# Performance work log

Hardware: AMD Instinct MI355X
Metric: run time of the kernel (lower is better)

Reference implementation:

```python
import jax, jax.numpy as jnp
import numpy as np

N = 8192
IN_F = 512
OUT_F = 256
ALPHA = 0.2          # LeakyReLU negative slope
MASK_VAL = -9e15     # same sentinel as the torch code


def setup_inputs() -> dict:
    key = jax.random.key(0)
    k1, k2, k3, k4, k5, k6 = jax.random.split(key, 6)
    inputs = jax.random.normal(k1, (N, IN_F), dtype=jnp.float32)
    # sparse-ish 0/1 dense adjacency (~avg degree 64)
    adj = (jax.random.uniform(k2, (N, N)) < (64.0 / N)).astype(jnp.float32)
    W = jax.random.normal(k3, (IN_F, OUT_F), dtype=jnp.float32) * (1.414 / np.sqrt(IN_F))
    a = jax.random.normal(k4, (2 * OUT_F, 1), dtype=jnp.float32) * 0.1
    W_gc = jax.random.normal(k5, (IN_F, OUT_F), dtype=jnp.float32) * (1.414 / np.sqrt(IN_F))
    b_gc = jax.random.normal(k6, (OUT_F,), dtype=jnp.float32) * 0.01
    return {"inputs": inputs, "adj": adj, "W": W, "a": a, "W_gc": W_gc, "b_gc": b_gc}


def reference(inputs, adj, W, a, W_gc, b_gc):
    # h: [n, F]
    h = inputs @ W
    F = h.shape[1]
    # Fused additive attention: e[i,j] = leaky_relu(a1.h_i + a2.h_j)
    # (mathematically identical to the repeat/cat construction in the source)
    f_src = h @ a[:F, 0]   # [n]
    f_dst = h @ a[F:, 0]   # [n]
    e = jax.nn.leaky_relu(f_src[:, None] + f_dst[None, :], negative_slope=ALPHA)  # [n, n]
    # masked row-softmax over neighbors
    att = jnp.where(adj > 0, e, MASK_VAL)
    att = jax.nn.softmax(att, axis=1)
    # dropout p=0.0 -> identity
    h_prime = att @ h  # [n, F]
    # optional dense graph-convolution branch (graph_convolve=True)
    gc = adj @ (inputs @ W_gc) + b_gc
    return h_prime + gc
```

## Files before the change

kernel.cpp:

```cpp
#include <hip/hip_runtime.h>
#include <hip/hip_bf16.h>
#include <math.h>

#define N_NODES 8192
#define IN_F    512
#define OUT_F   256
#define NCAT    512
#define ALPHA   0.2f
#define MAXDEG  512

typedef __attribute__((ext_vector_type(8))) short short8;
typedef __attribute__((ext_vector_type(4))) float f32x4;

static __device__ __forceinline__ short f2bf(float f) {
    union { float f; unsigned u; } v; v.f = f;
    unsigned r = v.u + 0x7fffu + ((v.u >> 16) & 1u);
    return (short)(r >> 16);
}
static __device__ __forceinline__ float bf2f(short s) {
    union { unsigned u; float f; } v;
    v.u = ((unsigned)(unsigned short)s) << 16;
    return v.f;
}

__global__ __launch_bounds__(512) void bt_pack(const float* __restrict__ W,
                                               const float* __restrict__ W_gc,
                                               short* __restrict__ Bt) {
    const int n = blockIdx.x;
    const int k = threadIdx.x;
    const int c = n >> 1;
    float v = (n & 1) ? W_gc[(size_t)k * OUT_F + c] : W[(size_t)k * OUT_F + c];
    Bt[(size_t)n * IN_F + k] = f2bf(v);
}

__global__ __launch_bounds__(256) void gemm_mfma(const float* __restrict__ A,
                                                 const short* __restrict__ Bt,
                                                 short* __restrict__ hcat) {
    __shared__ short As[128 * 32];
    __shared__ short Bs[128 * 32];

    const int tid  = threadIdx.x;
    const int m0   = blockIdx.y * 128;
    const int n0   = blockIdx.x * 128;
    const int wid  = tid >> 6;
    const int lane = tid & 63;
    const int wr   = wid >> 1;
    const int wc   = wid & 1;
    const int mh   = lane & 15;
    const int q    = lane >> 4;

    const int srow  = tid >> 1;
    const int shalf = tid & 1;

    const f32x4 vzero = {0.f, 0.f, 0.f, 0.f};
    f32x4 acc[4][4];
    #pragma unroll
    for (int i = 0; i < 4; i++)
        #pragma unroll
        for (int j = 0; j < 4; j++) acc[i][j] = vzero;

    const float* aga = A  + (size_t)(m0 + srow) * IN_F + shalf * 16;
    const short* bgb = Bt + (size_t)(n0 + srow) * IN_F + shalf * 16;
    short* asw = &As[srow * 32 + shalf * 16];
    short* bsw = &Bs[srow * 32 + shalf * 16];

    for (int k0 = 0; k0 < IN_F; k0 += 32) {
        const float4* a4 = (const float4*)(aga + k0);
        float4 x0 = a4[0], x1 = a4[1], x2 = a4[2], x3 = a4[3];
        const int4* b4 = (const int4*)(bgb + k0);
        int4 bv0 = b4[0], bv1 = b4[1];

        short8 p0, p1;
        p0[0] = f2bf(x0.x); p0[1] = f2bf(x0.y); p0[2] = f2bf(x0.z); p0[3] = f2bf(x0.w);
        p0[4] = f2bf(x1.x); p0[5] = f2bf(x1.y); p0[6] = f2bf(x1.z); p0[7] = f2bf(x1.w);
        p1[0] = f2bf(x2.x); p1[1] = f2bf(x2.y); p1[2] = f2bf(x2.z); p1[3] = f2bf(x2.w);
        p1[4] = f2bf(x3.x); p1[5] = f2bf(x3.y); p1[6] = f2bf(x3.z); p1[7] = f2bf(x3.w);

        __syncthreads();
        *(short8*)asw       = p0;
        *(short8*)(asw + 8) = p1;
        *(int4*)bsw         = bv0;
        *(int4*)(bsw + 8)   = bv1;
        __syncthreads();

        short8 af[4], bfm[4];
        #pragma unroll
        for (int i = 0; i < 4; i++) {
            af[i]  = *(const short8*)&As[(wr * 64 + i * 16 + mh) * 32 + q * 8];
            bfm[i] = *(const short8*)&Bs[(wc * 64 + i * 16 + mh) * 32 + q * 8];
        }
        #pragma unroll
        for (int mi = 0; mi < 4; mi++)
            #pragma unroll
            for (int ni = 0; ni < 4; ni++)
                acc[mi][ni] = __builtin_amdgcn_mfma_f32_16x16x32_bf16(
                    af[mi], bfm[ni], acc[mi][ni], 0, 0, 0);
    }

    #pragma unroll
    for (int mi = 0; mi < 4; mi++)
        #pragma unroll
        for (int ni = 0; ni < 4; ni++) {
            const int col   = n0 + wc * 64 + ni * 16 + mh;
            const int rbase = m0 + wr * 64 + mi * 16 + q * 4;
            f32x4 v = acc[mi][ni];
            #pragma unroll
            for (int r = 0; r < 4; r++)
                hcat[(size_t)(rbase + r) * NCAT + col] = f2bf(v[r]);
        }
}

__global__ __launch_bounds__(256) void compute_f(const short* __restrict__ hcat,
                                                 const float* __restrict__ a,
                                                 float* __restrict__ f_src,
                                                 float* __restrict__ f_dst) {
    const int row  = blockIdx.x * 4 + (threadIdx.x >> 6);
    const int lane = threadIdx.x & 63;
    const short* hr = hcat + (size_t)row * NCAT;
    float s1 = 0.f, s2 = 0.f;
    #pragma unroll
    for (int c = lane; c < OUT_F; c += 64) {
        float hv = bf2f(hr[2 * c]);
        s1 += hv * a[c];
        s2 += hv * a[OUT_F + c];
    }
    #pragma unroll
    for (int off = 32; off; off >>= 1) {
        s1 += __shfl_down(s1, off);
        s2 += __shfl_down(s2, off);
    }
    if (lane == 0) { f_src[row] = s1; f_dst[row] = s2; }
}

__global__ __launch_bounds__(256) void attn_row(const float* __restrict__ adj,
                                                const short* __restrict__ hcat,
                                                const float* __restrict__ f_src,
                                                const float* __restrict__ f_dst,
                                                const float* __restrict__ b_gc,
                                                float* __restrict__ out) {
    __shared__ int   s_idx[MAXDEG];
    __shared__ float s_w[MAXDEG];
    __shared__ float s_red[4];
    __shared__ int   s_count;

    const int row  = blockIdx.x;
    const int tid  = threadIdx.x;
    const int lane = tid & 63;
    const int wid  = tid >> 6;

    if (tid == 0) s_count = 0;
    __syncthreads();

    const float fs = f_src[row];
    const f32x4* arow4 = (const f32x4*)(adj + (size_t)row * N_NODES);

    f32x4 v[8];
    #pragma unroll
    for (int it = 0; it < 8; it++)
        v[it] = arow4[it * 256 + tid];

    float lloc = 0.f;
    #pragma unroll
    for (int it = 0; it < 8; it++) {
        int c4 = (v[it][0] > 0.f) + (v[it][1] > 0.f) +
                 (v[it][2] > 0.f) + (v[it][3] > 0.f);
        if (c4) {
            int pos = atomicAdd(&s_count, c4);
            const int j0 = (it * 256 + tid) * 4;
            #pragma unroll
            for (int i = 0; i < 4; i++) {
                if (v[it][i] > 0.f) {
                    float e = fs + f_dst[j0 + i];
                    e = (e > 0.f) ? e : ALPHA * e;
                    float w = __expf(e);
                    s_idx[pos] = j0 + i;
                    s_w[pos]   = w;
                    pos++;
                    lloc += w;
                }
            }
        }
    }
    #pragma unroll
    for (int off = 32; off; off >>= 1) lloc += __shfl_down(lloc, off);
    if (lane == 0) s_red[wid] = lloc;
    __syncthreads();

    const int   deg   = min(s_count, MAXDEG);
    const float l     = s_red[0] + s_red[1] + s_red[2] + s_red[3];
    const float inv_l = (deg > 0) ? 1.f / l : 0.f;

    const int u = lane >> 4;
    const int p = lane & 15;
    const short* hbase = hcat + wid * 128 + p * 8;

    float aa0 = 0.f, aa1 = 0.f, aa2 = 0.f, aa3 = 0.f;
    float gg0 = 0.f, gg1 = 0.f, gg2 = 0.f, gg3 = 0.f;
    #pragma unroll 4
    for (int k = u; k < deg; k += 4) {
        const int   j = s_idx[k];
        const float w = s_w[k];
        short8 hv = *(const short8*)(hbase + (size_t)j * NCAT);
        aa0 += w * bf2f(hv[0]); gg0 += bf2f(hv[1]);
        aa1 += w * bf2f(hv[2]); gg1 += bf2f(hv[3]);
        aa2 += w * bf2f(hv[4]); gg2 += bf2f(hv[5]);
        aa3 += w * bf2f(hv[6]); gg3 += bf2f(hv[7]);
    }
    aa0 += __shfl_down(aa0, 32); aa1 += __shfl_down(aa1, 32);
    aa2 += __shfl_down(aa2, 32); aa3 += __shfl_down(aa3, 32);
    gg0 += __shfl_down(gg0, 32); gg1 += __shfl_down(gg1, 32);
    gg2 += __shfl_down(gg2, 32); gg3 += __shfl_down(gg3, 32);
    aa0 += __shfl_down(aa0, 16); aa1 += __shfl_down(aa1, 16);
    aa2 += __shfl_down(aa2, 16); aa3 += __shfl_down(aa3, 16);
    gg0 += __shfl_down(gg0, 16); gg1 += __shfl_down(gg1, 16);
    gg2 += __shfl_down(gg2, 16); gg3 += __shfl_down(gg3, 16);

    if (u == 0) {
        const int col = wid * 64 + p * 4;
        const float4 bg = *(const float4*)(b_gc + col);
        float4 o;
        o.x = aa0 * inv_l + gg0 + bg.x;
        o.y = aa1 * inv_l + gg1 + bg.y;
        o.z = aa2 * inv_l + gg2 + bg.z;
        o.w = aa3 * inv_l + gg3 + bg.w;
        *(float4*)(out + (size_t)row * OUT_F + col) = o;
    }
}

extern "C" void kernel_launch(void* const* d_in, const int* in_sizes, int n_in,
                              void* d_out, int out_size, void* d_ws, size_t ws_size,
                              hipStream_t stream) {
    const float* inputs = (const float*)d_in[0];
    const float* adj    = (const float*)d_in[1];
    const float* W      = (const float*)d_in[2];
    const float* a      = (const float*)d_in[3];
    const float* W_gc   = (const float*)d_in[4];
    const float* b_gc   = (const float*)d_in[5];
    float* out = (float*)d_out;

    short* Bt    = (short*)d_ws;
    short* hcat  = Bt + (size_t)NCAT * IN_F;
    float* f_src = (float*)(hcat + (size_t)N_NODES * NCAT);
    float* f_dst = f_src + N_NODES;

    bt_pack<<<dim3(NCAT), dim3(IN_F), 0, stream>>>(W, W_gc, Bt);
    gemm_mfma<<<dim3(NCAT / 128, N_NODES / 128), 256, 0, stream>>>(inputs, Bt, hcat);
    compute_f<<<N_NODES / 4, 256, 0, stream>>>(hcat, a, f_src, f_dst);
    attn_row<<<N_NODES, 256, 0, stream>>>(adj, hcat, f_src, f_dst, b_gc, out);
}
```

Baseline: 424.1 us.

## Pre-pack inputs to bf16, shrink GEMM tiles, split attention weight pass, batch gathers

Adds a separate pass that converts the inputs to bf16 before the GEMM. The GEMM tile shrinks from 128x128 to 64x64, giving more blocks, and bt_pack is rewritten so its reads are coalesced. compute_f now does one vectorized load per lane. In attn_row, neighbor indices are collected first and the exp weights are computed in a separate balanced pass, so the per-thread divergent work goes away. The gather loop also issues 8 independent row loads at a time to hide latency. The costs are an extra kernel launch, extra memory traffic for the bf16 copy of the inputs, and less operand reuse per GEMM tile.

```diff
diff --git a/kernel.cpp b/kernel.cpp
--- a/kernel.cpp
+++ b/kernel.cpp
@@ -23,25 +23,38 @@
     return v.f;
 }
 
-__global__ __launch_bounds__(512) void bt_pack(const float* __restrict__ W,
+__global__ __launch_bounds__(256) void a_pack(const float* __restrict__ in,
+                                              short* __restrict__ Ab) {
+    const size_t idx = ((size_t)blockIdx.x * 256 + threadIdx.x) * 8;
+    const float4* p = (const float4*)(in + idx);
+    float4 x0 = p[0], x1 = p[1];
+    short8 o;
+    o[0] = f2bf(x0.x); o[1] = f2bf(x0.y); o[2] = f2bf(x0.z); o[3] = f2bf(x0.w);
+    o[4] = f2bf(x1.x); o[5] = f2bf(x1.y); o[6] = f2bf(x1.z); o[7] = f2bf(x1.w);
+    *(short8*)(Ab + idx) = o;
+}
+
+__global__ __launch_bounds__(256) void bt_pack(const float* __restrict__ W,
                                                const float* __restrict__ W_gc,
                                                short* __restrict__ Bt) {
-    const int n = blockIdx.x;
-    const int k = threadIdx.x;
-    const int c = n >> 1;
-    float v = (n & 1) ? W_gc[(size_t)k * OUT_F + c] : W[(size_t)k * OUT_F + c];
-    Bt[(size_t)n * IN_F + k] = f2bf(v);
-}
-
-__global__ __launch_bounds__(256) void gemm_mfma(const float* __restrict__ A,
+    const int idx = blockIdx.x * 256 + threadIdx.x;
+    const int k = idx >> 8;
+    const int c = idx & 255;
+    short w  = f2bf(W[idx]);
+    short wg = f2bf(W_gc[idx]);
+    Bt[(size_t)(2 * c)     * IN_F + k] = w;
+    Bt[(size_t)(2 * c + 1) * IN_F + k] = wg;
+}
+
+__global__ __launch_bounds__(256) void gemm_mfma(const short* __restrict__ Ab,
                                                  const short* __restrict__ Bt,
                                                  short* __restrict__ hcat) {
-    __shared__ short As[128 * 32];
-    __shared__ short Bs[128 * 32];
+    __shared__ short As[64 * 32];
+    __shared__ short Bs[64 * 32];
 
     const int tid  = threadIdx.x;
-    const int m0   = blockIdx.y * 128;
-    const int n0   = blockIdx.x * 128;
+    const int m0   = blockIdx.x * 64;
+    const int n0   = blockIdx.y * 64;
     const int wid  = tid >> 6;
     const int lane = tid & 63;
     const int wr   = wid >> 1;
@@ -49,60 +62,50 @@
     const int mh   = lane & 15;
     const int q    = lane >> 4;
 
-    const int srow  = tid >> 1;
-    const int shalf = tid & 1;
+    const int srow  = tid >> 2;
+    const int squad = (tid & 3) * 8;
 
     const f32x4 vzero = {0.f, 0.f, 0.f, 0.f};
-    f32x4 acc[4][4];
-    #pragma unroll
-    for (int i = 0; i < 4; i++)
-        #pragma unroll
-        for (int j = 0; j < 4; j++) acc[i][j] = vzero;
-
-    const float* aga = A  + (size_t)(m0 + srow) * IN_F + shalf * 16;
-    const short* bgb = Bt + (size_t)(n0 + srow) * IN_F + shalf * 16;
-    short* asw = &As[srow * 32 + shalf * 16];
-    short* bsw = &Bs[srow * 32 + shalf * 16];
+    f32x4 acc[2][2];
+    #pragma unroll
+    for (int i = 0; i < 2; i++)
+        #pragma unroll
+        for (int j = 0; j < 2; j++) acc[i][j] = vzero;
+
+    const short* ag = Ab + (size_t)(m0 + srow) * IN_F + squad;
+    const short* bg = Bt + (size_t)(n0 + srow) * IN_F + squad;
+    short* asw = &As[srow * 32 + squad];
+    short* bsw = &Bs[srow * 32 + squad];
 
     for (int k0 = 0; k0 < IN_F; k0 += 32) {
-        const float4* a4 = (const float4*)(aga + k0);
-        float4 x0 = a4[0], x1 = a4[1], x2 = a4[2], x3 = a4[3];
-        const int4* b4 = (const int4*)(bgb + k0);
-        int4 bv0 = b4[0], bv1 = b4[1];
-
-        short8 p0, p1;
-        p0[0] = f2bf(x0.x); p0[1] = f2bf(x0.y); p0[2] = f2bf(x0.z); p0[3] = f2bf(x0.w);
-        p0[4] = f2bf(x1.x); p0[5] = f2bf(x1.y); p0[6] = f2bf(x1.z); p0[7] = f2bf(x1.w);
-        p1[0] = f2bf(x2.x); p1[1] = f2bf(x2.y); p1[2] = f2bf(x2.z); p1[3] = f2bf(x2.w);
-        p1[4] = f2bf(x3.x); p1[5] = f2bf(x3.y); p1[6] = f2bf(x3.z); p1[7] = f2bf(x3.w);
+        int4 av = *(const int4*)(ag + k0);
+        int4 bv = *(const int4*)(bg + k0);
 
         __syncthreads();
-        *(short8*)asw       = p0;
-        *(short8*)(asw + 8) = p1;
-        *(int4*)bsw         = bv0;
-        *(int4*)(bsw + 8)   = bv1;
+        *(int4*)asw = av;
+        *(int4*)bsw = bv;
         __syncthreads();
 
-        short8 af[4], bfm[4];
-        #pragma unroll
-        for (int i = 0; i < 4; i++) {
-            af[i]  = *(const short8*)&As[(wr * 64 + i * 16 + mh) * 32 + q * 8];
-            bfm[i] = *(const short8*)&Bs[(wc * 64 + i * 16 + mh) * 32 + q * 8];
-        }
-        #pragma unroll
-        for (int mi = 0; mi < 4; mi++)
+        short8 af[2], bfm[2];
+        #pragma unroll
+        for (int i = 0; i < 2; i++) {
+            af[i]  = *(const short8*)&As[(wr * 32 + i * 16 + mh) * 32 + q * 8];
+            bfm[i] = *(const short8*)&Bs[(wc * 32 + i * 16 + mh) * 32 + q * 8];
+        }
+        #pragma unroll
+        for (int mi = 0; mi < 2; mi++)
             #pragma unroll
-            for (int ni = 0; ni < 4; ni++)
+            for (int ni = 0; ni < 2; ni++)
                 acc[mi][ni] = __builtin_amdgcn_mfma_f32_16x16x32_bf16(
                     af[mi], bfm[ni], acc[mi][ni], 0, 0, 0);
     }
 
     #pragma unroll
-    for (int mi = 0; mi < 4; mi++)
-        #pragma unroll
-        for (int ni = 0; ni < 4; ni++) {
-            const int col   = n0 + wc * 64 + ni * 16 + mh;
-            const int rbase = m0 + wr * 64 + mi * 16 + q * 4;
+    for (int mi = 0; mi < 2; mi++)
+        #pragma unroll
+        for (int ni = 0; ni < 2; ni++) {
+            const int col   = n0 + wc * 32 + ni * 16 + mh;
+            const int rbase = m0 + wr * 32 + mi * 16 + q * 4;
             f32x4 v = acc[mi][ni];
             #pragma unroll
             for (int r = 0; r < 4; r++)
@@ -116,14 +119,16 @@
                                                  float* __restrict__ f_dst) {
     const int row  = blockIdx.x * 4 + (threadIdx.x >> 6);
     const int lane = threadIdx.x & 63;
-    const short* hr = hcat + (size_t)row * NCAT;
-    float s1 = 0.f, s2 = 0.f;
-    #pragma unroll
-    for (int c = lane; c < OUT_F; c += 64) {
-        float hv = bf2f(hr[2 * c]);
-        s1 += hv * a[c];
-        s2 += hv * a[OUT_F + c];
-    }
+
+    short8 hv = *(const short8*)(hcat + (size_t)row * NCAT + lane * 8);
+    float4 a1 = *(const float4*)(a + lane * 4);
+    float4 a2 = *(const float4*)(a + OUT_F + lane * 4);
+
+    const float h0 = bf2f(hv[0]), h1 = bf2f(hv[2]);
+    const float h2 = bf2f(hv[4]), h3 = bf2f(hv[6]);
+    float s1 = h0 * a1.x + h1 * a1.y + h2 * a1.z + h3 * a1.w;
+    float s2 = h0 * a2.x + h1 * a2.y + h2 * a2.z + h3 * a2.w;
+
     #pragma unroll
     for (int off = 32; off; off >>= 1) {
         s1 += __shfl_down(s1, off);
@@ -151,7 +156,6 @@
     if (tid == 0) s_count = 0;
     __syncthreads();
 
-    const float fs = f_src[row];
     const f32x4* arow4 = (const f32x4*)(adj + (size_t)row * N_NODES);
 
     f32x4 v[8];
@@ -159,7 +163,6 @@
     for (int it = 0; it < 8; it++)
         v[it] = arow4[it * 256 + tid];
 
-    float lloc = 0.f;
     #pragma unroll
     for (int it = 0; it < 8; it++) {
         int c4 = (v[it][0] > 0.f) + (v[it][1] > 0.f) +
@@ -168,25 +171,29 @@
             int pos = atomicAdd(&s_count, c4);
             const int j0 = (it * 256 + tid) * 4;
             #pragma unroll
-            for (int i = 0; i < 4; i++) {
-                if (v[it][i] > 0.f) {
-                    float e = fs + f_dst[j0 + i];
-                    e = (e > 0.f) ? e : ALPHA * e;
-                    float w = __expf(e);
-                    s_idx[pos] = j0 + i;
-                    s_w[pos]   = w;
-                    pos++;
-                    lloc += w;
-                }
-            }
-        }
-    }
-    #pragma unroll
-    for (int off = 32; off; off >>= 1) lloc += __shfl_down(lloc, off);
-    if (lane == 0) s_red[wid] = lloc;
+            for (int i = 0; i < 4; i++)
+                if (v[it][i] > 0.f) s_idx[pos++] = j0 + i;
+        }
+    }
     __syncthreads();
 
-    const int   deg   = min(s_count, MAXDEG);
+    const int   deg = min(s_count, MAXDEG);
+    const float fs  = f_src[row];
+
+    float part = 0.f;
+    for (int t = tid; t < deg; t += 256) {
+        const int j = s_idx[t];
+        float e = fs + f_dst[j];
+        e = (e > 0.f) ? e : ALPHA * e;
+        const float w = __expf(e);
+        s_w[t] = w;
+        part += w;
+    }
+    #pragma unroll
+    for (int off = 32; off; off >>= 1) part += __shfl_down(part, off);
+    if (lane == 0) s_red[wid] = part;
+    __syncthreads();
+
     const float l     = s_red[0] + s_red[1] + s_red[2] + s_red[3];
     const float inv_l = (deg > 0) ? 1.f / l : 0.f;
 
@@ -196,8 +203,27 @@
 
     float aa0 = 0.f, aa1 = 0.f, aa2 = 0.f, aa3 = 0.f;
     float gg0 = 0.f, gg1 = 0.f, gg2 = 0.f, gg3 = 0.f;
+
+    int k = u;
+    for (; k + 28 < deg; k += 32) {
+        int   jj[8];
+        float ww[8];
+        #pragma unroll
+        for (int s = 0; s < 8; s++) { jj[s] = s_idx[k + s * 4]; ww[s] = s_w[k + s * 4]; }
+        short8 hv[8];
+        #pragma unroll
+        for (int s = 0; s < 8; s++)
+            hv[s] = *(const short8*)(hbase + (size_t)jj[s] * NCAT);
+        #pragma unroll
+        for (int s = 0; s < 8; s++) {
+            aa0 += ww[s] * bf2f(hv[s][0]); gg0 += bf2f(hv[s][1]);
+            aa1 += ww[s] * bf2f(hv[s][2]); gg1 += bf2f(hv[s][3]);
+            aa2 += ww[s] * bf2f(hv[s][4]); gg2 += bf2f(hv[s][5]);
+            aa3 += ww[s] * bf2f(hv[s][6]); gg3 += bf2f(hv[s][7]);
+        }
+    }
     #pragma unroll 4
-    for (int k = u; k < deg; k += 4) {
+    for (; k < deg; k += 4) {
         const int   j = s_idx[k];
         const float w = s_w[k];
         short8 hv = *(const short8*)(hbase + (size_t)j * NCAT);
@@ -206,6 +232,7 @@
         aa2 += w * bf2f(hv[4]); gg2 += bf2f(hv[5]);
         aa3 += w * bf2f(hv[6]); gg3 += bf2f(hv[7]);
     }
+
     aa0 += __shfl_down(aa0, 32); aa1 += __shfl_down(aa1, 32);
     aa2 += __shfl_down(aa2, 32); aa3 += __shfl_down(aa3, 32);
     gg0 += __shfl_down(gg0, 32); gg1 += __shfl_down(gg1, 32);
@@ -240,11 +267,13 @@
 
     short* Bt    = (short*)d_ws;
     short* hcat  = Bt + (size_t)NCAT * IN_F;
-    float* f_src = (float*)(hcat + (size_t)N_NODES * NCAT);
+    short* Ab    = hcat + (size_t)N_NODES * NCAT;
+    float* f_src = (float*)(Ab + (size_t)N_NODES * IN_F);
     float* f_dst = f_src + N_NODES;
 
-    bt_pack<<<dim3(NCAT), dim3(IN_F), 0, stream>>>(W, W_gc, Bt);
-    gemm_mfma<<<dim3(NCAT / 128, N_NODES / 128), 256, 0, stream>>>(inputs, Bt, hcat);
-    compute_f<<<N_NODES / 4, 256, 0, stream>>>(hcat, a, f_src, f_dst);
-    attn_row<<<N_NODES, 256, 0, stream>>>(adj, hcat, f_src, f_dst, b_gc, out);
-}
+    a_pack<<<dim3(N_NODES * IN_F / (8 * 256)), 256, 0, stream>>>(inputs, Ab);
+    bt_pack<<<dim3(IN_F * OUT_F / 256), 256, 0, stream>>>(W, W_gc, Bt);
+    gemm_mfma<<<dim3(N_NODES / 64, NCAT / 64), 256, 0, stream>>>(Ab, Bt, hcat);
+    compute_f<<<dim3(N_NODES / 4), 256, 0, stream>>>(hcat, a, f_src, f_dst);
+    attn_row<<<dim3(N_NODES), 256, 0, stream>>>(adj, hcat, f_src, f_dst, b_gc, out);
+}
```

New measurement: 405.5 us. -4.4%, faster.
